# Kernel tuning notes

Hardware: AMD Instinct MI355X
Metric: run time of the kernel (lower is better)

## Reference

```python
import jax, jax.numpy as jnp
import numpy as np

GRAPH_SIZE = 100000  # == N, used as scalar multiplier on Q


def setup_inputs() -> dict:
    key = jax.random.key(0)
    ks = jax.random.split(key, 10)
    N, D, K, C, S = 100000, 128, 10, 50000, 100
    inp = {
        "seeds_idx_pad": jax.random.randint(ks[0], (1, S), 0, N + 1),  # N = pad row
        "seeds_idx_num": jnp.full((1, 1), 50.0, dtype=jnp.float32),
        "candidates_idx": jax.random.randint(ks[1], (C,), 0, N),
        "all_nodes": jnp.arange(N),
        "mask": jnp.ones((N, 1), dtype=jnp.float32),
        "features": jax.random.normal(ks[2], (N, D), dtype=jnp.float32),
        "neigh_idx": jax.random.randint(ks[3], (N, K), 0, N),
        "W_self": jax.random.normal(ks[4], (D, D), dtype=jnp.float32) * 0.05,
        "W_neigh": jax.random.normal(ks[5], (D, D), dtype=jnp.float32) * 0.05,
        "W1": jax.random.normal(ks[6], (D, D + 1), dtype=jnp.float32) * 0.05,
        "W2": jax.random.normal(ks[7], (D, D + 1), dtype=jnp.float32) * 0.05,
        "W3": jax.random.normal(ks[8], (D, D + 1), dtype=jnp.float32) * 0.05,
    }
    return inp


def _sage(features, neigh_idx, all_nodes, mask, W_self, W_neigh):
    x = features[all_nodes]                 # [N, D]
    nb_mean = features[neigh_idx].mean(axis=1)  # [N, K, D] -> [N, D]
    h = jax.nn.relu(x @ W_self + nb_mean @ W_neigh)
    return h * mask                          # [N, D]


def reference(seeds_idx_pad, seeds_idx_num, candidates_idx, all_nodes, mask,
              features, neigh_idx, W_self, W_neigh, W1, W2, W3):
    D = features.shape[1]
    embedding = _sage(features, neigh_idx, all_nodes, mask, W_self, W_neigh)  # [N, D]
    embedding_pad = jnp.concatenate([embedding, jnp.zeros((1, D), embedding.dtype)], axis=0)
    seeds_emb = embedding_pad[seeds_idx_pad]                  # [1, S, D]
    seeds_mean = jax.nn.sigmoid((seeds_emb.sum(axis=1) / seeds_idx_num) @ W1)  # [1, D+1]
    global_mean = jax.nn.sigmoid(embedding.mean(axis=0)[None, :] @ W2)         # computed but unused, as in source
    candi_emb = jax.nn.sigmoid(embedding[candidates_idx] @ W3)                 # [C, D+1]
    Q = (1.0 - jnp.sum(candi_emb * seeds_mean, axis=1)) * GRAPH_SIZE           # [C]
    return Q
```

## Files before the change

### kernel.cpp

```cpp
#include <hip/hip_runtime.h>

#define D     128
#define DP1   129
#define KN    10
#define GSZ   100000.0f

typedef __attribute__((ext_vector_type(8))) _Float16 f16x8;
typedef __attribute__((ext_vector_type(4))) float f32x4;
typedef __attribute__((ext_vector_type(4))) unsigned uintx4;

#define MFMA16(a, b, c) __builtin_amdgcn_mfma_f32_16x16x32_f16((a), (b), (c), 0, 0, 0)

__device__ __forceinline__ float sigmoidf_(float x) {
    return 1.0f / (1.0f + __expf(-x));
}

__global__ __launch_bounds__(256) void prep_kernel(
    const float* __restrict__ features,
    const float* __restrict__ Wself, const float* __restrict__ Wneigh,
    const float* __restrict__ W3,
    const float* __restrict__ W1,
    const float* __restrict__ snum,
    const int*   __restrict__ seeds,
    const float* __restrict__ mask,
    const int*   __restrict__ neigh,
    unsigned short* __restrict__ featb,
    unsigned short* __restrict__ W2T,
    unsigned short* __restrict__ W3T,
    float*          __restrict__ srow,
    float*          __restrict__ smp,
    int*            __restrict__ done,
    int N, int S, int doW)
{
    int b = blockIdx.x;
    const int t = threadIdx.x;

    if (b < S) {
        __shared__ float xs[D], nb[D], sdot[D];
        __shared__ int lastFlag;

        const int node = seeds[b];
        if (node >= N || node < 0) {
            if (t < D) srow[b * D + t] = 0.f;
        } else {
            if (t < D) {
                xs[t] = features[(size_t)node * D + t];
                float a = 0.f;
                #pragma unroll
                for (int k = 0; k < KN; ++k)
                    a += features[(size_t)neigh[node * KN + k] * D + t];
                nb[t] = a * (1.0f / KN);
            }
            __syncthreads();
            if (t < D) {
                float h = 0.f;
                #pragma unroll 4
                for (int dp = 0; dp < D; ++dp)
                    h = fmaf(xs[dp], Wself[dp * D + t],
                             fmaf(nb[dp], Wneigh[dp * D + t], h));
                srow[b * D + t] = fmaxf(h, 0.f) * mask[node];
            }
        }
        __syncthreads();
        if (t == 0) {
            __threadfence();
            lastFlag = (atomicAdd(done, 1) == S - 1);
        }
        __syncthreads();
        if (lastFlag) {
            __threadfence();
            const int col = t & 127, hf = t >> 7;
            float a = 0.f;
            for (int b2 = hf; b2 < S; b2 += 2) a += srow[b2 * D + col];
            if (hf == 0) xs[col] = a; else nb[col] = a;
            __syncthreads();
            if (t < D) sdot[t] = (xs[t] + nb[t]) / snum[0];
            __syncthreads();
            if (t < DP1) {
                float acc = 0.f;
                #pragma unroll 4
                for (int dp = 0; dp < D; ++dp)
                    acc = fmaf(sdot[dp], W1[dp * DP1 + t], acc);
                smp[t] = sigmoidf_(acc);
            } else if (t < 144) {
                smp[t] = 0.0f;
            }
        }
        return;
    }
    b -= S;

    if (b < doW * 200) {
        const int u = b * 256 + t;
        if (u < 128 * 256) {
            int n = u >> 8, k = u & 255;
            float v = (k < 128) ? Wself[k * 128 + n] : Wneigh[(k - 128) * 128 + n];
            W2T[n * 256 + k] = __builtin_bit_cast(unsigned short, (_Float16)v);
        } else {
            int w = u - 128 * 256;
            if (w < 144 * 128) {
                int j = w >> 7, k = w & 127;
                float v = (j < DP1) ? W3[k * DP1 + j] : 0.0f;
                W3T[j * 128 + k] = __builtin_bit_cast(unsigned short, (_Float16)v);
            }
        }
        return;
    }
    b -= doW * 200;

    const int i = b * 256 + t;
    const int n8 = N * (D / 8);
    if (i < n8) {
        const float4 a = *(const float4*)(features + (size_t)i * 8);
        const float4 c = *(const float4*)(features + (size_t)i * 8 + 4);
        f16x8 v;
        v[0] = (_Float16)a.x; v[1] = (_Float16)a.y;
        v[2] = (_Float16)a.z; v[3] = (_Float16)a.w;
        v[4] = (_Float16)c.x; v[5] = (_Float16)c.y;
        v[6] = (_Float16)c.z; v[7] = (_Float16)c.w;
        *(f16x8*)(featb + (size_t)i * 8) = v;
    }
}

__global__ __launch_bounds__(256, 2) void fused_kernel(
    const int*            __restrict__ cand,
    const float*          __restrict__ mask,
    const unsigned short* __restrict__ featb,
    const int*            __restrict__ neigh,
    const unsigned short* __restrict__ W2T,
    const unsigned short* __restrict__ W3T,
    const float*          __restrict__ smp,
    float*                __restrict__ Q,
    int C)
{
    __shared__ unsigned short tile[16][256];
    __shared__ float msk[16];
    __shared__ float qred[4][16];

    const int lane  = threadIdx.x & 63;
    const int wv    = threadIdx.x >> 6;
    const int cbase = blockIdx.x * 16;

    const int g   = lane >> 4;
    const int n15 = lane & 15;

    {
        const int L   = lane & 15;
        const int grp = lane >> 4;
        const int m   = wv * 4 + grp;
        const int cc  = cbase + m;
        const int nd  = cand[(cc < C) ? cc : 0];
        if (L == 0) msk[m] = (cc < C) ? mask[nd] : 0.f;

        int rix[KN];
        #pragma unroll
        for (int k = 0; k < KN; ++k) rix[k] = neigh[nd * KN + k];

        const uintx4 xv = *(const uintx4*)(featb + (size_t)nd * D + L * 8);
        uintx4 vr[KN];
        #pragma unroll
        for (int k = 0; k < KN; ++k)
            vr[k] = *(const uintx4*)(featb + (size_t)rix[k] * D + L * 8);

        f16x8 s8 = __builtin_bit_cast(f16x8, vr[0]);
        #pragma unroll
        for (int k = 1; k < KN; ++k)
            s8 += __builtin_bit_cast(f16x8, vr[k]);
        const f16x8 nb8 = s8 * (f16x8)((_Float16)(1.0f / KN));

        const int sw = (m & 7) << 3;
        unsigned short* tw = &tile[0][0];
        *(uintx4*)(tw + m * 256 + ((L * 8) ^ sw))       = xv;
        *(uintx4*)(tw + m * 256 + ((128 + L * 8) ^ sw)) = __builtin_bit_cast(uintx4, nb8);
    }

    const int swr = (n15 & 7) << 3;
    const unsigned short* tp = &tile[0][0];

    __syncthreads();

    f16x8 afr[8];
    #pragma unroll
    for (int ks = 0; ks < 8; ++ks)
        afr[ks] = *reinterpret_cast<const f16x8*>(tp + n15 * 256 + ((ks * 32 + g * 8) ^ swr));

    f32x4 acc1[2];
    acc1[0] = (f32x4){0.f, 0.f, 0.f, 0.f};
    acc1[1] = (f32x4){0.f, 0.f, 0.f, 0.f};

    #pragma unroll
    for (int ks = 0; ks < 8; ++ks) {
        #pragma unroll
        for (int i = 0; i < 2; ++i) {
            const f16x8 b = *reinterpret_cast<const f16x8*>(
                W2T + ((wv * 2 + i) * 16 + n15) * 256 + ks * 32 + g * 8);
            acc1[i] = MFMA16(afr[ks], b, acc1[i]);
        }
    }

    float mr[4];
    #pragma unroll
    for (int r = 0; r < 4; ++r) mr[r] = msk[g * 4 + r];

    __syncthreads();

    #pragma unroll
    for (int i = 0; i < 2; ++i) {
        const f32x4 v = acc1[i];
        #pragma unroll
        for (int r = 0; r < 4; ++r) {
            const int m2 = g * 4 + r;
            tile[m2][(((wv * 2 + i) * 16 + n15)) ^ ((m2 & 7) << 3)] =
                __builtin_bit_cast(unsigned short, (_Float16)(fmaxf(v[r], 0.f) * mr[r]));
        }
    }
    __syncthreads();

    f16x8 ah[4];
    #pragma unroll
    for (int ks = 0; ks < 4; ++ks)
        ah[ks] = *reinterpret_cast<const f16x8*>(tp + n15 * 256 + ((ks * 32 + g * 8) ^ swr));

    const int jt0 = wv, jt1 = 4 + wv;
    f32x4 acc2[3];
    acc2[0] = (f32x4){0.f, 0.f, 0.f, 0.f};
    acc2[1] = (f32x4){0.f, 0.f, 0.f, 0.f};
    acc2[2] = (f32x4){0.f, 0.f, 0.f, 0.f};

    #pragma unroll
    for (int ks = 0; ks < 4; ++ks) {
        const f16x8 b0 = *reinterpret_cast<const f16x8*>(
            W3T + (jt0 * 16 + n15) * 128 + ks * 32 + g * 8);
        acc2[0] = MFMA16(ah[ks], b0, acc2[0]);
        const f16x8 b1 = *reinterpret_cast<const f16x8*>(
            W3T + (jt1 * 16 + n15) * 128 + ks * 32 + g * 8);
        acc2[1] = MFMA16(ah[ks], b1, acc2[1]);
        if (wv == 0) {
            const f16x8 b2 = *reinterpret_cast<const f16x8*>(
                W3T + (8 * 16 + n15) * 128 + ks * 32 + g * 8);
            acc2[2] = MFMA16(ah[ks], b2, acc2[2]);
        }
    }

    float qp[4] = {0.f, 0.f, 0.f, 0.f};
    {
        const float sm0 = smp[jt0 * 16 + n15];
        const float sm1 = smp[jt1 * 16 + n15];
        #pragma unroll
        for (int r = 0; r < 4; ++r) {
            qp[r] += sm0 * sigmoidf_(acc2[0][r]);
            qp[r] += sm1 * sigmoidf_(acc2[1][r]);
        }
        if (wv == 0) {
            const float sm2 = smp[8 * 16 + n15];
            #pragma unroll
            for (int r = 0; r < 4; ++r)
                qp[r] += sm2 * sigmoidf_(acc2[2][r]);
        }
    }
    #pragma unroll
    for (int off = 8; off >= 1; off >>= 1)
        #pragma unroll
        for (int r = 0; r < 4; ++r)
            qp[r] += __shfl_xor(qp[r], off);

    if (n15 == 0) {
        #pragma unroll
        for (int r = 0; r < 4; ++r)
            qred[wv][g * 4 + r] = qp[r];
    }
    __syncthreads();

    const int t = threadIdx.x;
    if (t < 16) {
        const float s = qred[0][t] + qred[1][t] + qred[2][t] + qred[3][t];
        const int cr = cbase + t;
        if (cr < C) Q[cr] = (1.0f - s) * GSZ;
    }
}

#define MCAND 8
__global__ __launch_bounds__(128) void cand_kernel(
    const int*   __restrict__ cand,
    const float* __restrict__ mask,
    const float* __restrict__ features,
    const int*   __restrict__ neigh,
    const float* __restrict__ Wself,
    const float* __restrict__ Wneigh,
    const float* __restrict__ W3,
    const float* __restrict__ sm,
    float*       __restrict__ Q,
    int C)
{
    const int c0 = blockIdx.x * MCAND;
    const int t  = threadIdx.x;

    __shared__ float z[2 * MCAND][D];
    __shared__ float h[MCAND][D];
    __shared__ float red1[MCAND][D];
    __shared__ float red2[MCAND][D];
    __shared__ float smsh[DP1];

    smsh[t] = sm[t];
    if (t == 0) smsh[D] = sm[D];

    float mskv[MCAND];
    #pragma unroll
    for (int m = 0; m < MCAND; ++m) {
        const int c    = c0 + m;
        const int node = (c < C) ? cand[c] : cand[0];
        mskv[m] = mask[node];
        z[m][t] = features[(size_t)node * D + t];
        float a = 0.f;
        #pragma unroll
        for (int k = 0; k < KN; ++k)
            a += features[(size_t)neigh[node * KN + k] * D + t];
        z[MCAND + m][t] = a * (1.0f / KN);
    }
    __syncthreads();

    float acc[MCAND];
    #pragma unroll
    for (int m = 0; m < MCAND; ++m) acc[m] = 0.f;
    for (int dp = 0; dp < D; dp += 4) {
        const float ws0 = Wself[(dp + 0) * D + t];
        const float ws1 = Wself[(dp + 1) * D + t];
        const float ws2 = Wself[(dp + 2) * D + t];
        const float ws3 = Wself[(dp + 3) * D + t];
        const float wn0 = Wneigh[(dp + 0) * D + t];
        const float wn1 = Wneigh[(dp + 1) * D + t];
        const float wn2 = Wneigh[(dp + 2) * D + t];
        const float wn3 = Wneigh[(dp + 3) * D + t];
        #pragma unroll
        for (int m = 0; m < MCAND; ++m) {
            const float4 xv = *(const float4*)&z[m][dp];
            const float4 nv = *(const float4*)&z[MCAND + m][dp];
            float a = acc[m];
            a = fmaf(xv.x, ws0, a); a = fmaf(xv.y, ws1, a);
            a = fmaf(xv.z, ws2, a); a = fmaf(xv.w, ws3, a);
            a = fmaf(nv.x, wn0, a); a = fmaf(nv.y, wn1, a);
            a = fmaf(nv.z, wn2, a); a = fmaf(nv.w, wn3, a);
            acc[m] = a;
        }
    }
    #pragma unroll
    for (int m = 0; m < MCAND; ++m)
        h[m][t] = fmaxf(acc[m], 0.f) * mskv[m];
    __syncthreads();

    #pragma unroll
    for (int m = 0; m < MCAND; ++m) acc[m] = 0.f;
    for (int dp = 0; dp < D; dp += 4) {
        const float w0 = W3[(dp + 0) * DP1 + t];
        const float w1 = W3[(dp + 1) * DP1 + t];
        const float w2 = W3[(dp + 2) * DP1 + t];
        const float w3 = W3[(dp + 3) * DP1 + t];
        #pragma unroll
        for (int m = 0; m < MCAND; ++m) {
            const float4 hv = *(const float4*)&h[m][dp];
            float a = acc[m];
            a = fmaf(hv.x, w0, a); a = fmaf(hv.y, w1, a);
            a = fmaf(hv.z, w2, a); a = fmaf(hv.w, w3, a);
            acc[m] = a;
        }
    }

    const float w128 = W3[t * DP1 + D];
    const float smt  = smsh[t];
    #pragma unroll
    for (int m = 0; m < MCAND; ++m) {
        red1[m][t] = smt * sigmoidf_(acc[m]);
        red2[m][t] = h[m][t] * w128;
    }
    __syncthreads();

    for (int off = 64; off > 0; off >>= 1) {
        if (t < off) {
            #pragma unroll
            for (int m = 0; m < MCAND; ++m) {
                red1[m][t] += red1[m][t + off];
                red2[m][t] += red2[m][t + off];
            }
        }
        __syncthreads();
    }

    if (t < MCAND && (c0 + t) < C) {
        const float dot = red1[t][0] + smsh[D] * sigmoidf_(red2[t][0]);
        Q[c0 + t] = (1.0f - dot) * GSZ;
    }
}

extern "C" void kernel_launch(void* const* d_in, const int* in_sizes, int n_in,
                              void* d_out, int out_size, void* d_ws, size_t ws_size,
                              hipStream_t stream)
{
    const int*   seeds    = (const int*)  d_in[0];
    const float* snum     = (const float*)d_in[1];
    const int*   cand     = (const int*)  d_in[2];
    const float* mask     = (const float*)d_in[4];
    const float* features = (const float*)d_in[5];
    const int*   neigh    = (const int*)  d_in[6];
    const float* Wself    = (const float*)d_in[7];
    const float* Wneigh   = (const float*)d_in[8];
    const float* W1       = (const float*)d_in[9];
    const float* W3       = (const float*)d_in[11];

    float* Q = (float*)d_out;

    const int S = in_sizes[0];
    const int C = in_sizes[2];
    const int N = in_sizes[3];

    char* ws = (char*)d_ws;
    float*          srow  = (float*)ws;
    float*          smp   = (float*)(ws + 57344);
    int*            done  = (int*)(ws + 58368);
    unsigned short* W2T   = (unsigned short*)(ws + 65536);
    unsigned short* W3T   = (unsigned short*)(ws + 131072);
    unsigned short* featb = (unsigned short*)(ws + 167936);
    const size_t need = 167936 + (size_t)N * D * 2;
    const bool small_ok = (size_t)S * D * 4 <= 57344;

    hipMemsetAsync(done, 0, sizeof(int), stream);

    if (ws_size >= need && small_ok && (N * D % 2048) == 0) {
        const int nFeatBlk = N * D / 2048;
        prep_kernel<<<S + 200 + nFeatBlk, 256, 0, stream>>>(
            features, Wself, Wneigh, W3, W1, snum, seeds, mask, neigh,
            featb, W2T, W3T, srow, smp, done, N, S, 1);
        const int nTiles = (C + 15) / 16;
        fused_kernel<<<nTiles, 256, 0, stream>>>(cand, mask, featb,
                                                 neigh, W2T, W3T, smp, Q, C);
    } else {
        prep_kernel<<<S, 256, 0, stream>>>(
            features, Wself, Wneigh, W3, W1, snum, seeds, mask, neigh,
            (unsigned short*)ws, (unsigned short*)ws, (unsigned short*)ws,
            srow, smp, done, N, S, 0);
        const int nblk = (C + MCAND - 1) / MCAND;
        cand_kernel<<<nblk, 128, 0, stream>>>(cand, mask, features,
                                              neigh, Wself, Wneigh, W3, smp, Q, C);
    }
}
```

Baseline: 99.26 us.

## Drop fp16 feature pre-conversion; gather fp32 features directly in fused kernel

```diff
diff --git a/kernel.cpp b/kernel.cpp
--- a/kernel.cpp
+++ b/kernel.cpp
@@ -13,6 +13,10 @@
 
 __device__ __forceinline__ float sigmoidf_(float x) {
     return 1.0f / (1.0f + __expf(-x));
+}
+__device__ __forceinline__ unsigned pkh(float lo, float hi) {
+    return (unsigned)__builtin_bit_cast(unsigned short, (_Float16)lo) |
+           ((unsigned)__builtin_bit_cast(unsigned short, (_Float16)hi) << 16);
 }
 
 __global__ __launch_bounds__(256) void prep_kernel(
@@ -24,7 +28,6 @@
     const int*   __restrict__ seeds,
     const float* __restrict__ mask,
     const int*   __restrict__ neigh,
-    unsigned short* __restrict__ featb,
     unsigned short* __restrict__ W2T,
     unsigned short* __restrict__ W3T,
     float*          __restrict__ srow,
@@ -104,28 +107,13 @@
                 W3T[j * 128 + k] = __builtin_bit_cast(unsigned short, (_Float16)v);
             }
         }
-        return;
-    }
-    b -= doW * 200;
-
-    const int i = b * 256 + t;
-    const int n8 = N * (D / 8);
-    if (i < n8) {
-        const float4 a = *(const float4*)(features + (size_t)i * 8);
-        const float4 c = *(const float4*)(features + (size_t)i * 8 + 4);
-        f16x8 v;
-        v[0] = (_Float16)a.x; v[1] = (_Float16)a.y;
-        v[2] = (_Float16)a.z; v[3] = (_Float16)a.w;
-        v[4] = (_Float16)c.x; v[5] = (_Float16)c.y;
-        v[6] = (_Float16)c.z; v[7] = (_Float16)c.w;
-        *(f16x8*)(featb + (size_t)i * 8) = v;
     }
 }
 
 __global__ __launch_bounds__(256, 2) void fused_kernel(
     const int*            __restrict__ cand,
     const float*          __restrict__ mask,
-    const unsigned short* __restrict__ featb,
+    const float*          __restrict__ features,
     const int*            __restrict__ neigh,
     const unsigned short* __restrict__ W2T,
     const unsigned short* __restrict__ W3T,
@@ -156,22 +144,30 @@
         #pragma unroll
         for (int k = 0; k < KN; ++k) rix[k] = neigh[nd * KN + k];
 
-        const uintx4 xv = *(const uintx4*)(featb + (size_t)nd * D + L * 8);
-        uintx4 vr[KN];
-        #pragma unroll
-        for (int k = 0; k < KN; ++k)
-            vr[k] = *(const uintx4*)(featb + (size_t)rix[k] * D + L * 8);
-
-        f16x8 s8 = __builtin_bit_cast(f16x8, vr[0]);
-        #pragma unroll
-        for (int k = 1; k < KN; ++k)
-            s8 += __builtin_bit_cast(f16x8, vr[k]);
-        const f16x8 nb8 = s8 * (f16x8)((_Float16)(1.0f / KN));
+        const float* fb = features + (size_t)L * 8;
+        const float4* xp = (const float4*)(fb + (size_t)nd * D);
+        const float4 xa = xp[0], xb = xp[1];
+
+        float4 sa = {0.f, 0.f, 0.f, 0.f}, sb = {0.f, 0.f, 0.f, 0.f};
+        #pragma unroll
+        for (int k = 0; k < KN; ++k) {
+            const float4* rp = (const float4*)(fb + (size_t)rix[k] * D);
+            const float4 va = rp[0], vb = rp[1];
+            sa.x += va.x; sa.y += va.y; sa.z += va.z; sa.w += va.w;
+            sb.x += vb.x; sb.y += vb.y; sb.z += vb.z; sb.w += vb.w;
+        }
+
+        uintx4 xv, nb;
+        xv[0] = pkh(xa.x, xa.y); xv[1] = pkh(xa.z, xa.w);
+        xv[2] = pkh(xb.x, xb.y); xv[3] = pkh(xb.z, xb.w);
+        const float inv = 1.0f / KN;
+        nb[0] = pkh(sa.x * inv, sa.y * inv); nb[1] = pkh(sa.z * inv, sa.w * inv);
+        nb[2] = pkh(sb.x * inv, sb.y * inv); nb[3] = pkh(sb.z * inv, sb.w * inv);
 
         const int sw = (m & 7) << 3;
         unsigned short* tw = &tile[0][0];
         *(uintx4*)(tw + m * 256 + ((L * 8) ^ sw))       = xv;
-        *(uintx4*)(tw + m * 256 + ((128 + L * 8) ^ sw)) = __builtin_bit_cast(uintx4, nb8);
+        *(uintx4*)(tw + m * 256 + ((128 + L * 8) ^ sw)) = nb;
     }
 
     const int swr = (n15 & 7) << 3;
@@ -413,29 +409,27 @@
     const int N = in_sizes[3];
 
     char* ws = (char*)d_ws;
-    float*          srow  = (float*)ws;
-    float*          smp   = (float*)(ws + 57344);
-    int*            done  = (int*)(ws + 58368);
-    unsigned short* W2T   = (unsigned short*)(ws + 65536);
-    unsigned short* W3T   = (unsigned short*)(ws + 131072);
-    unsigned short* featb = (unsigned short*)(ws + 167936);
-    const size_t need = 167936 + (size_t)N * D * 2;
+    float*          srow = (float*)ws;
+    float*          smp  = (float*)(ws + 57344);
+    int*            done = (int*)(ws + 58368);
+    unsigned short* W2T  = (unsigned short*)(ws + 65536);
+    unsigned short* W3T  = (unsigned short*)(ws + 131072);
+    const size_t need = 131072 + 144 * 128 * 2;
     const bool small_ok = (size_t)S * D * 4 <= 57344;
 
     hipMemsetAsync(done, 0, sizeof(int), stream);
 
-    if (ws_size >= need && small_ok && (N * D % 2048) == 0) {
-        const int nFeatBlk = N * D / 2048;
-        prep_kernel<<<S + 200 + nFeatBlk, 256, 0, stream>>>(
+    if (ws_size >= need && small_ok) {
+        prep_kernel<<<S + 200, 256, 0, stream>>>(
             features, Wself, Wneigh, W3, W1, snum, seeds, mask, neigh,
-            featb, W2T, W3T, srow, smp, done, N, S, 1);
+            W2T, W3T, srow, smp, done, N, S, 1);
         const int nTiles = (C + 15) / 16;
-        fused_kernel<<<nTiles, 256, 0, stream>>>(cand, mask, featb,
+        fused_kernel<<<nTiles, 256, 0, stream>>>(cand, mask, features,
                                                  neigh, W2T, W3T, smp, Q, C);
     } else {
         prep_kernel<<<S, 256, 0, stream>>>(
             features, Wself, Wneigh, W3, W1, snum, seeds, mask, neigh,
-            (unsigned short*)ws, (unsigned short*)ws, (unsigned short*)ws,
+            (unsigned short*)ws, (unsigned short*)ws,
             srow, smp, done, N, S, 0);
         const int nblk = (C + MCAND - 1) / MCAND;
         cand_kernel<<<nblk, 128, 0, stream>>>(cand, mask, features,
```

Measured after the change: 100.6 us. About the same (+1.4%).
